# Kernel tuning notes

Measured on AMD Instinct MI355X. Metric: run time of the kernel, lower is better.

Reference implementation:

```python
import jax, jax.numpy as jnp
import numpy as np

B, S, DIM, H, G, DH = 1, 2048, 2048, 16, 2, 128
L, D, LP, NSEL, W = 32, 16, 32, 16, 256   # compress len, stride, select block, top-k blocks, window
REP = H // G


def setup_inputs() -> dict:
    key = jax.random.key(0)
    ks = jax.random.split(key, 8)
    x = jax.random.normal(ks[0], (B, S, DIM), jnp.float32)
    inv = 1.0 / (10000.0 ** (jnp.arange(0, DH, 2, dtype=jnp.float32) / DH))
    ang = jnp.outer(jnp.arange(S, dtype=jnp.float32), inv)   # [S, DH//2]
    freqs_cos, freqs_sin = jnp.cos(ang), jnp.sin(ang)
    std = 0.02
    wq = jax.random.normal(ks[1], (DIM, H * DH), jnp.float32) * std
    wk = jax.random.normal(ks[2], (DIM, G * DH), jnp.float32) * std
    wv = jax.random.normal(ks[3], (DIM, G * DH), jnp.float32) * std
    wo = jax.random.normal(ks[4], (H * DH, DIM), jnp.float32) * std
    w_g = jax.random.normal(ks[5], (DH, 3), jnp.float32) * std
    return dict(x=x, freqs_cos=freqs_cos, freqs_sin=freqs_sin,
                wq=wq, wk=wk, wv=wv, wo=wo, w_g=w_g, start_pos=0)


def _rope(t, cos, sin):
    # t: [B,S,heads,DH]; complex pairs are consecutive elements (view_as_complex semantics)
    x0, x1 = t[..., 0::2], t[..., 1::2]
    c, s = cos[None, :, None, :], sin[None, :, None, :]
    return jnp.stack([x0 * c - x1 * s, x0 * s + x1 * c], axis=-1).reshape(t.shape)


def _nsa_forward(x, freqs_cos, freqs_sin, wq, wk, wv, wo, w_g):
    scale = DH ** -0.5
    q = (x @ wq).reshape(B, S, H, DH)
    k = (x @ wk).reshape(B, S, G, DH)
    v = (x @ wv).reshape(B, S, G, DH)
    q = _rope(q, freqs_cos, freqs_sin).reshape(B, S, G, REP, DH)
    k = _rope(k, freqs_cos, freqs_sin)

    tpos = jnp.arange(S)
    NEG = jnp.float32(-1e30)

    # ---- branch 1: compressed-block attention ----
    J = (S - L) // D + 1
    starts = jnp.arange(J) * D
    blk_idx = starts[:, None] + jnp.arange(L)[None, :]            # [J, L]
    k_cmp = k[:, blk_idx].mean(axis=2)                            # [B,J,G,DH]
    v_cmp = v[:, blk_idx].mean(axis=2)
    s_cmp = jnp.einsum('bsgrd,bjgd->bsgrj', q, k_cmp) * scale
    valid = (starts[None, :] + L - 1) <= tpos[:, None]            # [S, J]
    p_cmp = jax.nn.softmax(jnp.where(valid[None, :, None, None, :], s_cmp, NEG), axis=-1)
    p_cmp = jnp.where(valid.any(-1)[None, :, None, None, None], p_cmp, 0.0)
    o_cmp = jnp.einsum('bsgrj,bjgd->bsgrd', p_cmp, v_cmp)

    # ---- branch 2: top-n selected-block attention ----
    NB = S // LP
    sel_start = jnp.arange(NB) * LP
    # overlap of cmp block [j*D, j*D+L) with selection block [m*LP, m*LP+LP)
    ov = (starts[:, None] < sel_start[None, :] + LP) & (starts[:, None] + L > sel_start[None, :])
    imp = jnp.einsum('bsgrj,jm->bsgm', p_cmp, ov.astype(jnp.float32))   # sum over heads in group
    blk_causal = sel_start[None, :] <= tpos[:, None]                    # [S, NB]
    imp = jnp.where(blk_causal[None, :, None, :], imp, -jnp.inf)
    cur_blk = tpos // LP
    force = jax.nn.one_hot(cur_blk, NB) + jax.nn.one_hot(jnp.zeros_like(cur_blk), NB)
    imp = imp + force[None, :, None, :] * 1e9                           # always keep init + current block
    _, top_idx = jax.lax.top_k(imp, NSEL)                               # [B,S,G,NSEL]
    blk_mask = jax.nn.one_hot(top_idx, NB).sum(axis=-2) > 0             # [B,S,G,NB]
    tok_sel = jnp.repeat(blk_mask, LP, axis=-1)                         # [B,S,G,S]
    causal = tpos[:, None] >= tpos[None, :]                             # [S,S]

    s_full = jnp.einsum('bsgrd,btgd->bsgrt', q, k) * scale              # [B,S,G,R,S]
    m_sel = tok_sel[:, :, :, None, :] & causal[None, :, None, None, :]
    p_sel = jax.nn.softmax(jnp.where(m_sel, s_full, NEG), axis=-1)
    o_sel = jnp.einsum('bsgrt,btgd->bsgrd', p_sel, v)

    # ---- branch 3: sliding-window attention ----
    m_sw = causal & (tpos[None, :] > tpos[:, None] - W)
    p_sw = jax.nn.softmax(jnp.where(m_sw[None, :, None, None, :], s_full, NEG), axis=-1)
    o_sw = jnp.einsum('bsgrt,btgd->bsgrd', p_sw, v)

    # ---- learned gated combination ----
    g = jax.nn.sigmoid(jnp.einsum('bsgrd,de->bsgre', q, w_g))
    out = g[..., 0:1] * o_cmp + g[..., 1:2] * o_sel + g[..., 2:3] * o_sw
    return out.reshape(B, S, H * DH) @ wo


def reference(x, freqs_cos, freqs_sin, wq, wk, wv, wo, w_g, start_pos):
    return _nsa_forward(x, freqs_cos, freqs_sin, wq, wk, wv, wo, w_g)
```

## Files before the change

### kernel.cpp

```cpp
#include <hip/hip_runtime.h>
#include <cstddef>
#include <cstdint>
#include <math.h>

#define kS    2048
#define kDim  2048
#define kH    16
#define kG    2
#define kDH   128
#define kRep  8
#define kL    32
#define kDstr 16
#define kLP   32
#define kNSel 16
#define kW    256
#define kJ    127
#define kNB   64
#define kScale 0.08838834764831845f
#define kQT   4
#define kQF   8
#define kLDQ  2560

#define kKP   136
#define kVP   40

typedef __attribute__((ext_vector_type(4))) float f32x4;
typedef __attribute__((ext_vector_type(8))) __bf16 bf16x8;
typedef __attribute__((ext_vector_type(4))) __bf16 bf16x4;

__device__ __forceinline__ unsigned short f2bf(float f) {
  unsigned u = __float_as_uint(f);
  u += 0x7fff + ((u >> 16) & 1);
  return (unsigned short)(u >> 16);
}

#define GLDS16(src, dst)                                                     \
  __builtin_amdgcn_global_load_lds(                                          \
      (const __attribute__((address_space(1))) unsigned int*)(src),          \
      (__attribute__((address_space(3))) unsigned int*)(dst), 16, 0, 0)

__global__ void cast_bf16_kernel(const float* __restrict__ in,
                                 unsigned short* __restrict__ out, int n4) {
  int i = blockIdx.x * blockDim.x + threadIdx.x;
  if (i >= n4) return;
  float4 v = reinterpret_cast<const float4*>(in)[i];
  ushort4 o;
  o.x = f2bf(v.x); o.y = f2bf(v.y); o.z = f2bf(v.z); o.w = f2bf(v.w);
  reinterpret_cast<ushort4*>(out)[i] = o;
}

__global__ __launch_bounds__(256) void transpose_cast_kernel(
    const float* __restrict__ in, int ldin, unsigned short* __restrict__ out,
    int rows, int cols) {
  __shared__ float tile[32][33];
  const int bx = blockIdx.x * 32;
  const int by = blockIdx.y * 32;
  const int tx = threadIdx.x & 31;
  const int ty = threadIdx.x >> 5;
#pragma unroll
  for (int i = 0; i < 32; i += 8)
    tile[ty + i][tx] = in[(size_t)(by + ty + i) * ldin + bx + tx];
  __syncthreads();
#pragma unroll
  for (int i = 0; i < 32; i += 8)
    out[(size_t)(bx + ty + i) * rows + by + tx] = f2bf(tile[tx][ty + i]);
}

__global__ __launch_bounds__(256) void transpose_weights_kernel(
    const float* __restrict__ wq, const float* __restrict__ wk,
    const float* __restrict__ wv, const float* __restrict__ wo,
    unsigned short* __restrict__ wqT, unsigned short* __restrict__ wkT,
    unsigned short* __restrict__ wvT, unsigned short* __restrict__ woT) {
  int b = blockIdx.x;
  const float* in;
  unsigned short* out;
  int rows, cols, rel;
  if (b < 4096)      { in = wq; out = wqT; rows = 2048; cols = 2048; rel = b; }
  else if (b < 4608) { in = wk; out = wkT; rows = 2048; cols = 256;  rel = b - 4096; }
  else if (b < 5120) { in = wv; out = wvT; rows = 2048; cols = 256;  rel = b - 4608; }
  else               { in = wo; out = woT; rows = 2048; cols = 2048; rel = b - 5120; }
  const int nbx = cols >> 5;
  const int bx = (rel % nbx) * 32;
  const int by = (rel / nbx) * 32;
  __shared__ float tile[32][33];
  const int tx = threadIdx.x & 31;
  const int ty = threadIdx.x >> 5;
#pragma unroll
  for (int i = 0; i < 32; i += 8)
    tile[ty + i][tx] = in[(size_t)(by + ty + i) * cols + bx + tx];
  __syncthreads();
#pragma unroll
  for (int i = 0; i < 32; i += 8)
    out[(size_t)(bx + ty + i) * rows + by + tx] = f2bf(tile[tx][ty + i]);
}

__global__ __launch_bounds__(512) void gemm_bf16_kernel(
    const unsigned short* __restrict__ A,
    const unsigned short* __restrict__ Bt,
    float* __restrict__ C, int M, int N, int ldc, int K) {
  __shared__ __align__(16) unsigned short As[64 * 32];
  __shared__ __align__(16) unsigned short Bs[128 * 32];
  const int t = threadIdx.x;
  const int lane = t & 63;
  const int wid = t >> 6;
  const int wr = wid >> 2;
  const int wc = wid & 3;
  const int lhi = lane >> 4, llo = lane & 15;
  const size_t row0 = (size_t)blockIdx.y * 64;
  const size_t col0 = (size_t)blockIdx.x * 128;

  f32x4 acc[2][2];
#pragma unroll
  for (int m = 0; m < 2; ++m)
#pragma unroll
    for (int n = 0; n < 2; ++n) acc[m][n] = f32x4{0.f, 0.f, 0.f, 0.f};

  const int ra = t >> 2, ka = (t & 3) * 8;
  const int rb = t >> 2, kb2 = (t & 3) * 8;

  for (int k0 = 0; k0 < K; k0 += 32) {
    if (t < 256)
      GLDS16(A + (row0 + ra) * (size_t)K + k0 + ka, As + t * 8);
    GLDS16(Bt + (col0 + rb) * (size_t)K + k0 + kb2, Bs + t * 8);
    __syncthreads();
    bf16x8 af[2], bfr[2];
#pragma unroll
    for (int m = 0; m < 2; ++m)
      af[m] = *reinterpret_cast<const bf16x8*>(&As[(wr * 32 + m * 16 + llo) * 32 + lhi * 8]);
#pragma unroll
    for (int n = 0; n < 2; ++n)
      bfr[n] = *reinterpret_cast<const bf16x8*>(&Bs[(wc * 32 + n * 16 + llo) * 32 + lhi * 8]);
#pragma unroll
    for (int m = 0; m < 2; ++m)
#pragma unroll
      for (int n = 0; n < 2; ++n)
        acc[m][n] = __builtin_amdgcn_mfma_f32_16x16x32_bf16(af[m], bfr[n], acc[m][n], 0, 0, 0);
    __syncthreads();
  }
#pragma unroll
  for (int m = 0; m < 2; ++m)
#pragma unroll
    for (int n = 0; n < 2; ++n)
#pragma unroll
      for (int j = 0; j < 4; ++j) {
        size_t r = row0 + wr * 32 + m * 16 + lhi * 4 + j;
        size_t c = col0 + wc * 32 + n * 16 + llo;
        C[r * (size_t)ldc + c] = acc[m][n][j];
      }
}

__global__ void rope2_kernel(float* __restrict__ qkv,
                             const float* __restrict__ fc,
                             const float* __restrict__ fsn,
                             unsigned short* __restrict__ qb,
                             unsigned short* __restrict__ kb) {
  int idx = blockIdx.x * blockDim.x + threadIdx.x;
  const int totq = kS * kH * 64;
  float* tb;
  unsigned short* outb;
  int nheads, ldout;
  if (idx < totq) {
    tb = qkv; outb = qb; nheads = kH; ldout = kDim;
  } else {
    idx -= totq;
    tb = qkv + kDim; outb = kb; nheads = kG; ldout = kG * kDH;
  }
  int i = idx & 63;
  int h = (idx >> 6) % nheads;
  int s = idx / (64 * nheads);
  float c = fc[s * 64 + i];
  float sn = fsn[s * 64 + i];
  float* p = tb + (size_t)s * kLDQ + h * kDH + 2 * i;
  float x0 = p[0], x1 = p[1];
  float r0 = x0 * c - x1 * sn;
  float r1 = x0 * sn + x1 * c;
  p[0] = r0;
  p[1] = r1;
  unsigned short* o = outb + (size_t)s * ldout + h * kDH + 2 * i;
  o[0] = f2bf(r0);
  o[1] = f2bf(r1);
}

__global__ void pool_kernel(const float* __restrict__ qkv,
                            float* __restrict__ kcT,
                            unsigned short* __restrict__ vcT) {
  int idx = blockIdx.x * blockDim.x + threadIdx.x;
  if (idx >= 128 * kG * kDH) return;
  int d = idx & 127;
  int g = (idx >> 7) & 1;
  int j = idx >> 8;
  float sk = 0.f, sv = 0.f;
  if (j < kJ) {
    for (int l = 0; l < kL; ++l) {
      size_t row = (size_t)(j * kDstr + l) * kLDQ;
      sk += qkv[row + kDim + g * kDH + d];
      sv += qkv[row + kDim + kG * kDH + g * kDH + d];
    }
    sk *= (1.f / 32.f);
    sv *= (1.f / 32.f);
  }
  size_t o = ((size_t)(g * 128 + d)) * 128 + j;
  kcT[o] = sk;
  vcT[o] = f2bf(sv);
}

__global__ __launch_bounds__(256) void cmp_attn_kernel(
    const float* __restrict__ qkv, const float* __restrict__ kcT,
    const unsigned short* __restrict__ vcT,
    const float* __restrict__ wg,
    float* __restrict__ oc, float* __restrict__ gates,
    unsigned long long* __restrict__ selmask) {
  __shared__ float qst[128][36];
  __shared__ float pT [128][36];
  __shared__ __align__(16) char ubuf[32 * 132 * 4];
  float (*kvt)[132] = reinterpret_cast<float(*)[132]>(ubuf);
  unsigned short (*pTb)[136] = reinterpret_cast<unsigned short(*)[136]>(ubuf);

  const int b = blockIdx.x;
  const int g = b & 1;
  const int s0 = (b >> 1) * kQT;
  const int t = threadIdx.x;
  const int ty = t >> 5;
  const int tx = t & 31;

  {
    int row = t & 31;
    int dl = (t >> 5) * 16;
    const float* src = qkv + (size_t)(s0 + (row >> 3)) * kLDQ +
                       (g * kRep + (row & 7)) * kDH + dl;
#pragma unroll
    for (int i = 0; i < 4; ++i) {
      float4 v = *reinterpret_cast<const float4*>(src + i * 4);
      qst[dl + i * 4 + 0][row] = v.x;
      qst[dl + i * 4 + 1][row] = v.y;
      qst[dl + i * 4 + 2][row] = v.z;
      qst[dl + i * 4 + 3][row] = v.w;
    }
  }
  __syncthreads();

  float S[4][4];
#pragma unroll
  for (int rr = 0; rr < 4; ++rr)
#pragma unroll
    for (int jj = 0; jj < 4; ++jj) S[rr][jj] = 0.f;

  for (int dt = 0; dt < 4; ++dt) {
    {
      const float* base = kcT + (size_t)(g * 128 + dt * 32) * 128;
#pragma unroll
      for (int i = 0; i < 4; ++i) {
        int s = t + i * 256;
        int dd = s >> 5;
        int j4 = s & 31;
        *reinterpret_cast<float4*>(&kvt[dd][j4 * 4]) =
            *reinterpret_cast<const float4*>(base + dd * 128 + j4 * 4);
      }
    }
    __syncthreads();
#pragma unroll
    for (int kk = 0; kk < 32; ++kk) {
      float4 a = *reinterpret_cast<const float4*>(&qst[dt * 32 + kk][ty * 4]);
      float4 bb = *reinterpret_cast<const float4*>(&kvt[kk][tx * 4]);
      float av[4] = {a.x, a.y, a.z, a.w};
      float bv[4] = {bb.x, bb.y, bb.z, bb.w};
#pragma unroll
      for (int rr = 0; rr < 4; ++rr)
#pragma unroll
        for (int jj = 0; jj < 4; ++jj)
          S[rr][jj] = fmaf(av[rr], bv[jj], S[rr][jj]);
    }
    __syncthreads();
  }

#pragma unroll
  for (int rr = 0; rr < 4; ++rr) {
    int row = ty * 4 + rr;
    int s = s0 + (row >> 3);
    int jmax = (s >= kL - 1) ? ((s - (kL - 1)) >> 4) : -1;
#pragma unroll
    for (int jj = 0; jj < 4; ++jj) {
      int j = tx * 4 + jj;
      pT[j][row] = (j <= jmax && j < kJ) ? S[rr][jj] * kScale : -1e30f;
    }
  }
  __syncthreads();

  {
    int row = t >> 3;
    int l = t & 7;
    int s = s0 + (row >> 3);
    if (s < kL - 1) {
#pragma unroll
      for (int i = 0; i < 16; ++i) pT[l + i * 8][row] = 0.f;
    } else {
      float vals[16];
      float mx = -INFINITY;
#pragma unroll
      for (int i = 0; i < 16; ++i) {
        vals[i] = pT[l + i * 8][row];
        mx = fmaxf(mx, vals[i]);
      }
      mx = fmaxf(mx, __shfl_xor(mx, 1));
      mx = fmaxf(mx, __shfl_xor(mx, 2));
      mx = fmaxf(mx, __shfl_xor(mx, 4));
      float sm = 0.f;
#pragma unroll
      for (int i = 0; i < 16; ++i) {
        vals[i] = __expf(vals[i] - mx);
        sm += vals[i];
      }
      sm += __shfl_xor(sm, 1);
      sm += __shfl_xor(sm, 2);
      sm += __shfl_xor(sm, 4);
      float inv = 1.f / sm;
#pragma unroll
      for (int i = 0; i < 16; ++i) pT[l + i * 8][row] = vals[i] * inv;
    }
  }
  __syncthreads();

  {
    int row = t >> 3;
    int l = t & 7;
#pragma unroll
    for (int i = 0; i < 16; ++i)
      pTb[row][l + i * 8] = f2bf(pT[l + i * 8][row]);
  }
  {
    int qq = t >> 6;
    int m = t & 63;
    int s = s0 + qq;
    int mcur = s >> 5;
    float im;
    if (m > mcur) {
      im = -INFINITY;
    } else {
      im = 0.f;
#pragma unroll
      for (int r = 0; r < 8; ++r) {
        int row = qq * 8 + r;
        float sp = (2 * m - 1 >= 0) ? pT[2 * m - 1][row] : 0.f;
        sp += pT[2 * m][row];
        if (2 * m + 1 < kJ) sp += pT[2 * m + 1][row];
        im += sp;
      }
      if (m == 0) im += 1e9f;
      if (m == mcur) im += 1e9f;
    }
    bool taken = false;
    unsigned long long mask = 0ull;
    for (int it = 0; it < kNSel; ++it) {
      float cv = taken ? -INFINITY : im;
      int ci = taken ? 64 : m;
#pragma unroll
      for (int off = 1; off < 64; off <<= 1) {
        float ov = __shfl_xor(cv, off);
        int oi = __shfl_xor(ci, off);
        if (ov > cv || (ov == cv && oi < ci)) { cv = ov; ci = oi; }
      }
      mask |= 1ull << ci;
      if (m == ci) taken = true;
    }
    if (m == 0) selmask[(size_t)s * 2 + g] = mask;
  }
  if (t < 192) {
    int task = t >> 1;
    int p = t & 1;
    int row = task / 3;
    int e = task - row * 3;
    int sQ = s0 + (row >> 3);
    int r = row & 7;
    const float* qr = qkv + (size_t)sQ * kLDQ + (g * kRep + r) * kDH + p * 64;
    float acc = 0.f;
#pragma unroll
    for (int i = 0; i < 16; ++i) {
      float4 v = *reinterpret_cast<const float4*>(qr + i * 4);
      int d = p * 64 + i * 4;
      acc = fmaf(v.x, wg[d * 3 + e], acc);
      acc = fmaf(v.y, wg[(d + 1) * 3 + e], acc);
      acc = fmaf(v.z, wg[(d + 2) * 3 + e], acc);
      acc = fmaf(v.w, wg[(d + 3) * 3 + e], acc);
    }
    acc += __shfl_xor(acc, 1);
    if (p == 0)
      gates[((size_t)(sQ * 2 + g) * kRep + r) * 3 + e] = 1.f / (1.f + __expf(-acc));
  }
  __syncthreads();

  {
    const int lane = t & 63;
    const int wv = t >> 6;
    const int lo = lane & 15, hi = lane >> 4;
    f32x4 acc[2][2];
#pragma unroll
    for (int rt = 0; rt < 2; ++rt)
#pragma unroll
      for (int dt2 = 0; dt2 < 2; ++dt2) acc[rt][dt2] = f32x4{0.f, 0.f, 0.f, 0.f};
#pragma unroll
    for (int ks = 0; ks < 4; ++ks) {
      bf16x8 pf[2], vf[2];
#pragma unroll
      for (int rt = 0; rt < 2; ++rt)
        pf[rt] = *reinterpret_cast<const bf16x8*>(&pTb[rt * 16 + lo][ks * 32 + hi * 8]);
#pragma unroll
      for (int dt2 = 0; dt2 < 2; ++dt2)
        vf[dt2] = *reinterpret_cast<const bf16x8*>(
            vcT + ((size_t)(g * 128 + wv * 32 + dt2 * 16 + lo)) * 128 + ks * 32 + hi * 8);
#pragma unroll
      for (int rt = 0; rt < 2; ++rt)
#pragma unroll
        for (int dt2 = 0; dt2 < 2; ++dt2)
          acc[rt][dt2] = __builtin_amdgcn_mfma_f32_16x16x32_bf16(vf[dt2], pf[rt], acc[rt][dt2], 0, 0, 0);
    }
#pragma unroll
    for (int rt = 0; rt < 2; ++rt) {
      int qrow = rt * 16 + lo;
      size_t base = ((size_t)(s0 + (qrow >> 3)) * kH + g * kRep + (qrow & 7)) * kDH;
#pragma unroll
      for (int dt2 = 0; dt2 < 2; ++dt2) {
        int d0 = wv * 32 + dt2 * 16 + hi * 4;
#pragma unroll
        for (int jj = 0; jj < 4; ++jj)
          oc[base + d0 + jj] = acc[rt][dt2][jj];
      }
    }
  }
}

template <int MODE>
__device__ __forceinline__ void attn_tile3(
    const unsigned short* __restrict__ Ksb, const unsigned short* __restrict__ VTb,
    const bf16x8 (&qf)[4], __bf16* Psw,
    int tb, unsigned selw, int wv, int lo, int hi, int s0,
    f32x4 (&O)[8], float& mst, float& lst) {
  f32x4 S0 = f32x4{0.f, 0.f, 0.f, 0.f};
  f32x4 S1 = f32x4{0.f, 0.f, 0.f, 0.f};
  __builtin_amdgcn_s_setprio(1);
#pragma unroll
  for (int ds = 0; ds < 4; ++ds) {
    bf16x8 a0 = *reinterpret_cast<const bf16x8*>(&Ksb[lo * kKP + ds * 32 + hi * 8]);
    bf16x8 a1 = *reinterpret_cast<const bf16x8*>(&Ksb[(16 + lo) * kKP + ds * 32 + hi * 8]);
    S0 = __builtin_amdgcn_mfma_f32_16x16x32_bf16(a0, qf[ds], S0, 0, 0, 0);
    S1 = __builtin_amdgcn_mfma_f32_16x16x32_bf16(a1, qf[ds], S1, 0, 0, 0);
  }
  __builtin_amdgcn_s_setprio(0);
  const int qloc = wv * 2 + (lo >> 3);
  const int s_row = s0 + qloc;
  const bool selq = (MODE == 1) || (((selw >> qloc) & 1u) != 0);
  float sv[2][4];
#pragma unroll
  for (int j = 0; j < 4; ++j) { sv[0][j] = S0[j]; sv[1][j] = S1[j]; }
#pragma unroll
  for (int tf = 0; tf < 2; ++tf)
#pragma unroll
    for (int j = 0; j < 4; ++j) {
      int tok = tb + tf * 16 + hi * 4 + j;
      bool ok = selq && (tok <= s_row) && (MODE == 0 || tok > s_row - kW);
      sv[tf][j] = ok ? sv[tf][j] * kScale : -1e30f;
    }
  float pm = sv[0][0];
#pragma unroll
  for (int tf = 0; tf < 2; ++tf)
#pragma unroll
    for (int j = 0; j < 4; ++j) pm = fmaxf(pm, sv[tf][j]);
  pm = fmaxf(pm, __shfl_xor(pm, 16));
  pm = fmaxf(pm, __shfl_xor(pm, 32));
  if (__any(pm > mst + 8.f)) {
    float mn = fmaxf(mst, pm);
    float f = __expf(mst - mn);
#pragma unroll
    for (int df = 0; df < 8; ++df)
#pragma unroll
      for (int j = 0; j < 4; ++j) O[df][j] *= f;
    lst *= f;
    mst = mn;
  }
  float lacc = 0.f;
#pragma unroll
  for (int tf = 0; tf < 2; ++tf) {
    bf16x4 pk;
#pragma unroll
    for (int j = 0; j < 4; ++j) {
      float e = __expf(sv[tf][j] - mst);
      lacc += e;
      pk[j] = (__bf16)e;
    }
    *reinterpret_cast<bf16x4*>(&Psw[lo * 40 + tf * 16 + hi * 4]) = pk;
  }
  lst += lacc;
  bf16x8 pfrag = *reinterpret_cast<const bf16x8*>(&Psw[lo * 40 + hi * 8]);
  __builtin_amdgcn_s_setprio(1);
#pragma unroll
  for (int df = 0; df < 8; ++df) {
    bf16x8 vf = *reinterpret_cast<const bf16x8*>(&VTb[(df * 16 + lo) * kVP + hi * 8]);
    O[df] = __builtin_amdgcn_mfma_f32_16x16x32_bf16(vf, pfrag, O[df], 0, 0, 0);
  }
  __builtin_amdgcn_s_setprio(0);
}

__global__ __launch_bounds__(256) void fused_attn_kernel(
    const unsigned short* __restrict__ qb, const unsigned short* __restrict__ kb,
    const unsigned short* __restrict__ vT, const float* __restrict__ ocp,
    const float* __restrict__ gts,
    const unsigned long long* __restrict__ selmask,
    unsigned short* __restrict__ preb) {
  __shared__ __align__(16) unsigned short Ks[2][32 * kKP];
  __shared__ __align__(16) unsigned short VTs[2][128 * kVP];
  __shared__ __align__(16) __bf16 Ps[4][16 * 40];
  __shared__ unsigned long long qm[kQF];
  __shared__ unsigned char selbits[kNB];
  __shared__ unsigned char blist[kNB];
  __shared__ int nsel_sh;

  const int bid = blockIdx.x;
  const int g = bid & 1;
  const int idx = bid >> 1;
  const int qt = (idx < 128) ? idx : 383 - idx;
  const int s0 = qt * kQF;
  const int t = threadIdx.x;
  const int lane = t & 63;
  const int wv = t >> 6;
  const int lo = lane & 15, hi = lane >> 4;

  int kBase[3], vBase[3];
#pragma unroll
  for (int ii = 0; ii < 3; ++ii) {
    int s = t + ii * 256;
    int r = s / 17, c = s - r * 17;
    if (c > 15) c = 0;
    kBase[ii] = r * 256 + g * 128 + c * 8;
    int r2 = s / 5, c2 = s - r2 * 5;
    if (c2 > 3) c2 = 0;
    vBase[ii] = (g * 128 + r2) * 2048 + c2 * 8;
  }
  auto STAGE = [&](int tb, unsigned short* Ksb, unsigned short* VTb) {
#pragma unroll
    for (int ii = 0; ii < 3; ++ii) {
      if (ii < 2 || t < 32)
        GLDS16(kb + (size_t)tb * 256 + kBase[ii], Ksb + (t + ii * 256) * 8);
      if (ii < 2 || t < 128)
        GLDS16(vT + (size_t)vBase[ii] + tb, VTb + (t + ii * 256) * 8);
    }
  };

  const int qrow = wv * 16 + lo;
  const int s_q = s0 + (qrow >> 3);
  const int hd = qrow & 7;
  bf16x8 qf[4];
  {
    const unsigned short* src = qb + ((size_t)s_q * 16 + g * 8 + hd) * 128 + hi * 8;
#pragma unroll
    for (int ds = 0; ds < 4; ++ds)
      qf[ds] = *reinterpret_cast<const bf16x8*>(src + ds * 32);
  }
  if (t < kQF) {
    int sQ = s0 + t;
    unsigned long long mm = selmask[(size_t)sQ * 2 + g];
    mm &= ((2ull << (sQ >> 5)) - 1ull);
    qm[t] = mm;
  }
  __syncthreads();
  if (t < kNB) {
    unsigned b = 0;
    for (int ql = 0; ql < kQF; ++ql)
      b |= (unsigned)((qm[ql] >> t) & 1ull) << ql;
    selbits[t] = (unsigned char)b;
  }
  if (t == 0) {
    unsigned long long u = 0;
    for (int ql = 0; ql < kQF; ++ql) u |= qm[ql];
    int n = 0;
    for (int m = 0; m < kNB; ++m)
      if ((u >> m) & 1ull) blist[n++] = (unsigned char)m;
    nsel_sh = n;
  }
  __syncthreads();

  __bf16* Psw = &Ps[wv][0];

  f32x4 O1[8], O2[8];
#pragma unroll
  for (int df = 0; df < 8; ++df) O1[df] = f32x4{0.f, 0.f, 0.f, 0.f};
  float mst = -INFINITY, lst = 0.f;

  const int nsel = nsel_sh;
  int cur = 0;
  STAGE((int)blist[0] * 32, Ks[0], VTs[0]);
  __syncthreads();
  for (int i = 0; i < nsel; ++i) {
    if (i + 1 < nsel)
      STAGE((int)blist[i + 1] * 32, Ks[cur ^ 1], VTs[cur ^ 1]);
    int b = blist[i];
    attn_tile3<0>(Ks[cur], VTs[cur], qf, Psw, b * 32, selbits[b], wv, lo, hi, s0,
                  O1, mst, lst);
    __syncthreads();
    cur ^= 1;
  }
  const int hi_t = s0 >> 5;
  const int lo_t = (s0 > 255) ? ((s0 - 255) >> 5) : 0;
  STAGE(hi_t * 32, Ks[cur], VTs[cur]);
  float g0v, g2v;
  {
    const float* gp = gts + ((size_t)(s_q * 2 + g) * 8 + hd) * 3;
    g0v = gp[0];
    g2v = gp[2];
    float lt = lst;
    lt += __shfl_xor(lt, 16);
    lt += __shfl_xor(lt, 32);
    float f = gp[1] / lt;
#pragma unroll
    for (int df = 0; df < 8; ++df)
#pragma unroll
      for (int j = 0; j < 4; ++j) O1[df][j] *= f;
  }
  mst = -INFINITY;
  lst = 0.f;
#pragma unroll
  for (int df = 0; df < 8; ++df) O2[df] = f32x4{0.f, 0.f, 0.f, 0.f};
  __syncthreads();

  for (int tt = hi_t; tt >= lo_t; --tt) {
    if (tt - 1 >= lo_t)
      STAGE((tt - 1) * 32, Ks[cur ^ 1], VTs[cur ^ 1]);
    attn_tile3<1>(Ks[cur], VTs[cur], qf, Psw, tt * 32, 0u, wv, lo, hi, s0,
                  O2, mst, lst);
    __syncthreads();
    cur ^= 1;
  }

  {
    float lt = lst;
    lt += __shfl_xor(lt, 16);
    lt += __shfl_xor(lt, 32);
    float f2 = g2v / lt;
    size_t base = ((size_t)s_q * 16 + g * 8 + hd) * 128;
#pragma unroll
    for (int df = 0; df < 8; ++df) {
      int d0 = df * 16 + hi * 4;
      float4 ocv = *reinterpret_cast<const float4*>(&ocp[base + d0]);
      ushort4 w;
      w.x = f2bf(g0v * ocv.x + O1[df][0] + f2 * O2[df][0]);
      w.y = f2bf(g0v * ocv.y + O1[df][1] + f2 * O2[df][1]);
      w.z = f2bf(g0v * ocv.z + O1[df][2] + f2 * O2[df][2]);
      w.w = f2bf(g0v * ocv.w + O1[df][3] + f2 * O2[df][3]);
      *reinterpret_cast<ushort4*>(&preb[base + d0]) = w;
    }
  }
}

extern "C" void kernel_launch(void* const* d_in, const int* in_sizes, int n_in,
                              void* d_out, int out_size, void* d_ws, size_t ws_size,
                              hipStream_t stream) {
  (void)in_sizes; (void)n_in; (void)out_size; (void)ws_size;
  const float* x  = (const float*)d_in[0];
  const float* fc = (const float*)d_in[1];
  const float* fs = (const float*)d_in[2];
  const float* wq = (const float*)d_in[3];
  const float* wk = (const float*)d_in[4];
  const float* wv = (const float*)d_in[5];
  const float* wo = (const float*)d_in[6];
  const float* wg = (const float*)d_in[7];
  float* out = (float*)d_out;

  float* qkv  = (float*)d_ws;
  float* kcT  = qkv + (size_t)kS * kLDQ;
  float* oc   = kcT + 256 * 128;
  float* gts  = oc + kS * kH * kDH;
  unsigned long long* selmask = (unsigned long long*)(gts + kS * kG * kRep * 3);
  unsigned short* xb   = (unsigned short*)(selmask + kS * kG);
  unsigned short* wqT  = xb + kS * kDim;
  unsigned short* wkT  = wqT + (kH * kDH) * kDim;
  unsigned short* wvT  = wkT + (kG * kDH) * kDim;
  unsigned short* woT  = wvT + (kG * kDH) * kDim;
  unsigned short* preb = woT + kDim * (kH * kDH);
  unsigned short* kb   = preb + kS * kDim;
  unsigned short* vT   = kb + kS * kG * kDH;
  unsigned short* vcTb = vT + kS * kG * kDH;
  unsigned short* qbuf = xb;

  dim3 blk256(256);
  dim3 blk512(512);
  cast_bf16_kernel<<<kS * kDim / 4 / 256, blk256, 0, stream>>>(x, xb, kS * kDim / 4);
  transpose_weights_kernel<<<9216, blk256, 0, stream>>>(
      wq, wk, wv, wo, wqT, wkT, wvT, woT);
  gemm_bf16_kernel<<<dim3(kLDQ / 128, kS / 64), blk512, 0, stream>>>(
      xb, wqT, qkv, kS, kLDQ, kLDQ, kDim);
  rope2_kernel<<<(kS * kH * 64 + kS * kG * 64) / 256, blk256, 0, stream>>>(
      qkv, fc, fs, qbuf, kb);
  transpose_cast_kernel<<<dim3(kG * kDH / 32, kS / 32), blk256, 0, stream>>>(
      qkv + kDim + kG * kDH, kLDQ, vT, kS, kG * kDH);
  pool_kernel<<<128, blk256, 0, stream>>>(qkv, kcT, vcTb);
  cmp_attn_kernel<<<kS / kQT * kG, blk256, 0, stream>>>(qkv, kcT, vcTb, wg, oc, gts, selmask);
  fused_attn_kernel<<<kS / kQF * kG, blk256, 0, stream>>>(qbuf, kb, vT, oc, gts, selmask, preb);
  gemm_bf16_kernel<<<dim3(kDim / 128, kS / 64), blk512, 0, stream>>>(
      preb, woT, out, kS, kDim, kDim, kH * kDH);
}
```

Before: 248.1 us.

## Merge selected and sliding-window tile loops into one two-tile-per-barrier pipeline

Builds a single tile list that holds the selected blocks followed by the sliding-window tiles, and processes two tiles per double-buffered stage so each barrier covers twice the work. The separate loop transition, with its extra stage and barrier, goes away, and the gate values are loaded once at the start. This doubles the shared memory used for K/V staging, which may reduce occupancy, and adds branching inside the per-tile processing.

```diff
diff --git a/kernel.cpp b/kernel.cpp
--- a/kernel.cpp
+++ b/kernel.cpp
@@ -505,13 +505,13 @@
     const float* __restrict__ gts,
     const unsigned long long* __restrict__ selmask,
     unsigned short* __restrict__ preb) {
-  __shared__ __align__(16) unsigned short Ks[2][32 * kKP];
-  __shared__ __align__(16) unsigned short VTs[2][128 * kVP];
+  __shared__ __align__(16) unsigned short Ks[2][2][32 * kKP];
+  __shared__ __align__(16) unsigned short VTs[2][2][128 * kVP];
   __shared__ __align__(16) __bf16 Ps[4][16 * 40];
   __shared__ unsigned long long qm[kQF];
   __shared__ unsigned char selbits[kNB];
-  __shared__ unsigned char blist[kNB];
-  __shared__ int nsel_sh;
+  __shared__ unsigned char tlist[kNB + 12];
+  __shared__ int nsel_sh, ntiles_sh;
 
   const int bid = blockIdx.x;
   const int g = bid & 1;
@@ -548,11 +548,14 @@
   const int s_q = s0 + (qrow >> 3);
   const int hd = qrow & 7;
   bf16x8 qf[4];
+  float g0v, g1v, g2v;
   {
     const unsigned short* src = qb + ((size_t)s_q * 16 + g * 8 + hd) * 128 + hi * 8;
 #pragma unroll
     for (int ds = 0; ds < 4; ++ds)
       qf[ds] = *reinterpret_cast<const bf16x8*>(src + ds * 32);
+    const float* gp = gts + ((size_t)(s_q * 2 + g) * 8 + hd) * 3;
+    g0v = gp[0]; g1v = gp[1]; g2v = gp[2];
   }
   if (t < kQF) {
     int sQ = s0 + t;
@@ -572,59 +575,61 @@
     for (int ql = 0; ql < kQF; ++ql) u |= qm[ql];
     int n = 0;
     for (int m = 0; m < kNB; ++m)
-      if ((u >> m) & 1ull) blist[n++] = (unsigned char)m;
+      if ((u >> m) & 1ull) tlist[n++] = (unsigned char)m;
     nsel_sh = n;
+    int hi_t = s0 >> 5;
+    int lo_t = (s0 > 255) ? ((s0 - 255) >> 5) : 0;
+    for (int tt = hi_t; tt >= lo_t; --tt) tlist[n++] = (unsigned char)tt;
+    ntiles_sh = n;
   }
   __syncthreads();
 
   __bf16* Psw = &Ps[wv][0];
+  const int nsel = nsel_sh;
+  const int NT = ntiles_sh;
 
   f32x4 O1[8], O2[8];
 #pragma unroll
-  for (int df = 0; df < 8; ++df) O1[df] = f32x4{0.f, 0.f, 0.f, 0.f};
+  for (int df = 0; df < 8; ++df) {
+    O1[df] = f32x4{0.f, 0.f, 0.f, 0.f};
+    O2[df] = f32x4{0.f, 0.f, 0.f, 0.f};
+  }
   float mst = -INFINITY, lst = 0.f;
 
-  const int nsel = nsel_sh;
+  auto PROCESS = [&](int i, const unsigned short* Ksb, const unsigned short* VTb) {
+    int tb = (int)tlist[i] * 32;
+    if (i < nsel) {
+      attn_tile3<0>(Ksb, VTb, qf, Psw, tb, selbits[tlist[i]], wv, lo, hi, s0,
+                    O1, mst, lst);
+      if (i == nsel - 1) {
+        float lt = lst;
+        lt += __shfl_xor(lt, 16);
+        lt += __shfl_xor(lt, 32);
+        float f = g1v / lt;
+#pragma unroll
+        for (int df = 0; df < 8; ++df)
+#pragma unroll
+          for (int j = 0; j < 4; ++j) O1[df][j] *= f;
+        mst = -INFINITY;
+        lst = 0.f;
+      }
+    } else {
+      attn_tile3<1>(Ksb, VTb, qf, Psw, tb, 0u, wv, lo, hi, s0, O2, mst, lst);
+    }
+  };
+
   int cur = 0;
-  STAGE((int)blist[0] * 32, Ks[0], VTs[0]);
-  __syncthreads();
-  for (int i = 0; i < nsel; ++i) {
-    if (i + 1 < nsel)
-      STAGE((int)blist[i + 1] * 32, Ks[cur ^ 1], VTs[cur ^ 1]);
-    int b = blist[i];
-    attn_tile3<0>(Ks[cur], VTs[cur], qf, Psw, b * 32, selbits[b], wv, lo, hi, s0,
-                  O1, mst, lst);
-    __syncthreads();
-    cur ^= 1;
-  }
-  const int hi_t = s0 >> 5;
-  const int lo_t = (s0 > 255) ? ((s0 - 255) >> 5) : 0;
-  STAGE(hi_t * 32, Ks[cur], VTs[cur]);
-  float g0v, g2v;
-  {
-    const float* gp = gts + ((size_t)(s_q * 2 + g) * 8 + hd) * 3;
-    g0v = gp[0];
-    g2v = gp[2];
-    float lt = lst;
-    lt += __shfl_xor(lt, 16);
-    lt += __shfl_xor(lt, 32);
-    float f = gp[1] / lt;
-#pragma unroll
-    for (int df = 0; df < 8; ++df)
-#pragma unroll
-      for (int j = 0; j < 4; ++j) O1[df][j] *= f;
-  }
-  mst = -INFINITY;
-  lst = 0.f;
-#pragma unroll
-  for (int df = 0; df < 8; ++df) O2[df] = f32x4{0.f, 0.f, 0.f, 0.f};
-  __syncthreads();
-
-  for (int tt = hi_t; tt >= lo_t; --tt) {
-    if (tt - 1 >= lo_t)
-      STAGE((tt - 1) * 32, Ks[cur ^ 1], VTs[cur ^ 1]);
-    attn_tile3<1>(Ks[cur], VTs[cur], qf, Psw, tt * 32, 0u, wv, lo, hi, s0,
-                  O2, mst, lst);
+  STAGE((int)tlist[0] * 32, Ks[0][0], VTs[0][0]);
+  if (1 < NT) STAGE((int)tlist[1] * 32, Ks[0][1], VTs[0][1]);
+  __syncthreads();
+  for (int base = 0; base < NT; base += 2) {
+    if (base + 2 < NT)
+      STAGE((int)tlist[base + 2] * 32, Ks[cur ^ 1][0], VTs[cur ^ 1][0]);
+    if (base + 3 < NT)
+      STAGE((int)tlist[base + 3] * 32, Ks[cur ^ 1][1], VTs[cur ^ 1][1]);
+    PROCESS(base, Ks[cur][0], VTs[cur][0]);
+    if (base + 1 < NT)
+      PROCESS(base + 1, Ks[cur][1], VTs[cur][1]);
     __syncthreads();
     cur ^= 1;
   }
```

Result: slower. 271.2 us (+9.3%).
